# Optimization experiments

Hardware: AMD Instinct MI355X
Metric: run time of the kernel (lower is better)

Reference implementation:

```python
import jax, jax.numpy as jnp
import numpy as np

# Phi-2 config
B, S = 4, 1024            # batch, seq_len (uniform prefill)
T = B * S                 # total tokens
HID = 2560
H = 32                    # attention heads
D = HID // H              # head_size = 80
ROT = int(0.4 * D)        # partial rotary dim = 32
THETA = 10000.0
SCALE = D ** -0.5
NUM_SLOTS = 2 * T


def setup_inputs() -> dict:
    key = jax.random.key(0)
    ks = jax.random.split(key, 6)
    hidden_states = jax.random.normal(ks[0], (T, HID), jnp.float32) * 0.02
    # true rope tables: positions restart per sequence
    pos = jnp.tile(jnp.arange(S, dtype=jnp.float32), B)                 # [T]
    inv_freq = 1.0 / (THETA ** (jnp.arange(0, ROT, 2, dtype=jnp.float32) / ROT))  # [ROT/2]
    freqs = pos[:, None] * inv_freq[None, :]                            # [T, ROT/2]
    cos, sin = jnp.cos(freqs), jnp.sin(freqs)
    slots = jnp.arange(T, dtype=jnp.int32)
    kv_cache_k = jnp.zeros((NUM_SLOTS, H, D), jnp.float32)
    kv_cache_v = jnp.zeros((NUM_SLOTS, H, D), jnp.float32)
    qkv_w = jax.random.normal(ks[1], (3 * HID, HID), jnp.float32) * 0.02
    qkv_b = jax.random.normal(ks[2], (3 * HID,), jnp.float32) * 0.02
    dense_w = jax.random.normal(ks[3], (HID, HID), jnp.float32) * 0.02
    dense_b = jax.random.normal(ks[4], (HID,), jnp.float32) * 0.02
    return {"hidden_states": hidden_states, "cos": cos, "sin": sin, "slots": slots,
            "kv_cache_k": kv_cache_k, "kv_cache_v": kv_cache_v,
            "qkv_w": qkv_w, "qkv_b": qkv_b, "dense_w": dense_w, "dense_b": dense_b}


def _partial_rope(x, cos, sin):
    # x: [T, H, D]; rotate-half rope on the first ROT dims only
    x1 = x[..., : ROT // 2]
    x2 = x[..., ROT // 2 : ROT]
    c = cos[:, None, :]  # [T,1,ROT/2]
    s = sin[:, None, :]
    rot = jnp.concatenate([x1 * c - x2 * s, x1 * s + x2 * c], axis=-1)
    return jnp.concatenate([rot, x[..., ROT:]], axis=-1)


def reference(hidden_states, cos, sin, slots, kv_cache_k, kv_cache_v,
              qkv_w, qkv_b, dense_w, dense_b):
    # fused QKV projection
    qkv = hidden_states @ qkv_w.T + qkv_b                 # [T, 3*HID]
    q = qkv[:, :HID].reshape(T, H, D)
    k = qkv[:, HID:2 * HID].reshape(T, H, D)
    v = qkv[:, 2 * HID:].reshape(T, H, D)
    # partial rotary on q and k
    q = _partial_rope(q, cos, sin)
    k = _partial_rope(k, cos, sin)
    # KV-cache write (reshape_and_cache)
    kc = kv_cache_k.at[slots].set(k)
    vc = kv_cache_v.at[slots].set(v)
    # causal flash-attention (prefill path), uniform seq lengths
    qb = q.reshape(B, S, H, D)
    kb = k.reshape(B, S, H, D)
    vb = v.reshape(B, S, H, D)
    scores = jnp.einsum("bqhd,bkhd->bhqk", qb, kb) * SCALE  # [B,H,S,S]
    causal = jnp.tril(jnp.ones((S, S), bool))
    scores = jnp.where(causal[None, None], scores, jnp.finfo(scores.dtype).min)
    probs = jax.nn.softmax(scores, axis=-1)
    attn = jnp.einsum("bhqk,bkhd->bqhd", probs, vb).reshape(T, HID)
    out = attn @ dense_w.T + dense_b                       # [T, HID]
    return out, kc, vc
```

## Files before the change

kernel.cpp:

```cpp
#include <hip/hip_runtime.h>

#define SEQ    1024
#define NBAT   4
#define TTOK   4096
#define HIDN   2560
#define NQKV   7680
#define NHEAD  32
#define DHEAD  80
#define NSLOT  8192
#define SCALE_F 0.111803398874989485f
#define LOG2E_F 1.4426950408889634f

typedef float  f32x4  __attribute__((ext_vector_type(4)));
typedef __bf16 bf16x8 __attribute__((ext_vector_type(8)));
typedef short  s16x8  __attribute__((ext_vector_type(8)));
typedef short  s16x4  __attribute__((ext_vector_type(4)));
typedef ushort u16x4  __attribute__((ext_vector_type(4)));

typedef __attribute__((address_space(3))) void lds_v;
typedef __attribute__((address_space(1))) void glb_v;

__device__ __forceinline__ void gload16(const void* g, void* l) {
  __builtin_amdgcn_global_load_lds((glb_v*)g, (lds_v*)l, 16, 0, 0);
}

__device__ __forceinline__ f32x4 mfma16(s16x8 a, s16x8 b, f32x4 c) {
  return __builtin_amdgcn_mfma_f32_16x16x32_bf16(
      __builtin_bit_cast(bf16x8, a), __builtin_bit_cast(bf16x8, b), c, 0, 0, 0);
}

__device__ __forceinline__ ushort f2bf(float f) {
  uint u = __builtin_bit_cast(uint, f);
  u += 0x7fffu + ((u >> 16) & 1u);
  return (ushort)(u >> 16);
}
__device__ __forceinline__ float bf2f(ushort h) {
  uint u = (uint)h << 16;
  return __builtin_bit_cast(float, u);
}

__global__ __launch_bounds__(256)
void cvt_f32_bf16(const float* __restrict__ src, ushort* __restrict__ dst, int n) {
  int i = (blockIdx.x * 256 + threadIdx.x) * 4;
  const int stride = gridDim.x * 256 * 4;
  for (; i < n; i += stride) {
    float4 v = *(const float4*)(src + i);
    u16x4 o = { f2bf(v.x), f2bf(v.y), f2bf(v.z), f2bf(v.w) };
    *(u16x4*)(dst + i) = o;
  }
}

template<int OUT_BF16>
__global__ __launch_bounds__(512, 2)
void gemm8p(const ushort* __restrict__ A, const ushort* __restrict__ B,
            const float* __restrict__ bias, void* __restrict__ Cout,
            int M, int N, int K, int GX) {
  __shared__ ushort sA[3][256 * 64];
  __shared__ ushort sB[2][256 * 64];
  const int tid = threadIdx.x;
  const int l   = tid & 63;
  const int w   = tid >> 6;
  const int wm  = w >> 2, wn = w & 3;
  const int r   = l & 15,  g = l >> 4;

  const int nwg = gridDim.x;
  const int cpx = nwg >> 3;
  const int fl  = blockIdx.x;
  const int sw  = (fl & 7) * cpx + (fl >> 3);
  const int bx  = sw % GX, by = sw / GX;
  const int m0  = by * 256, n0 = bx * 256;
  const int NT  = K >> 6;

  const int srow = w * 16 + (l >> 3);
  const int scol = ((l & 7) ^ (l >> 3)) * 8;
  const ushort* Ab = A + (size_t)(m0 + srow) * K + scol;
  const ushort* Bb = B + (size_t)(n0 + srow) * K + scol;
  const size_t r8   = (size_t)8 * K;
  const size_t r128 = (size_t)128 * K;

#define STG_A(t_, h_, buf_) { \
    const ushort* gp = Ab + (size_t)(t_) * 64 + (size_t)(h_) * r128; \
    char* lp = (char*)(&sA[buf_][0]) + ((h_) * 128 + w * 16) * 128; \
    gload16(gp, lp); gload16(gp + r8, lp + 1024); }
#define STG_B(t_, h_, buf_) { \
    const ushort* gp = Bb + (size_t)(t_) * 64 + (size_t)(h_) * r128; \
    char* lp = (char*)(&sB[buf_][0]) + ((h_) * 128 + w * 16) * 128; \
    gload16(gp, lp); gload16(gp + r8, lp + 1024); }

  const int kswz = (r & 7) * 8;
  const int c0 = (g * 8) ^ kswz;
  const int c1 = (32 + g * 8) ^ kswz;
  const int arow = (wm * 128 + r) * 64;
  const int brow = (wn * 64 + r) * 64;

  f32x4 acc[8][4];
#pragma unroll
  for (int m = 0; m < 8; m++)
#pragma unroll
    for (int n = 0; n < 4; n++) { f32x4 z = {0.f,0.f,0.f,0.f}; acc[m][n] = z; }

  STG_A(0, 0, 0); STG_A(0, 1, 0);
  STG_B(0, 0, 0); STG_B(0, 1, 0);
  STG_A(1, 0, 1); STG_A(1, 1, 1);
  asm volatile("s_waitcnt vmcnt(4)" ::: "memory");
  __builtin_amdgcn_sched_barrier(0);
  __builtin_amdgcn_s_barrier();

#define MFMA_Q(q_) \
    __builtin_amdgcn_s_setprio(1); \
    _Pragma("unroll") \
    for (int n = 0; n < 4; n++) { \
      acc[2*(q_)  ][n] = mfma16(x0, b0[n], acc[2*(q_)  ][n]); \
      acc[2*(q_)  ][n] = mfma16(x1, b1[n], acc[2*(q_)  ][n]); \
      acc[2*(q_)+1][n] = mfma16(y0, b0[n], acc[2*(q_)+1][n]); \
      acc[2*(q_)+1][n] = mfma16(y1, b1[n], acc[2*(q_)+1][n]); \
    } \
    __builtin_amdgcn_s_setprio(0);

#define LOAD_A(m0_, m1_) \
    x0 = *(const s16x8*)&cA[arow + (m0_) * 1024 + c0]; \
    x1 = *(const s16x8*)&cA[arow + (m0_) * 1024 + c1]; \
    y0 = *(const s16x8*)&cA[arow + (m1_) * 1024 + c0]; \
    y1 = *(const s16x8*)&cA[arow + (m1_) * 1024 + c1];

  int bA = 0;
#pragma unroll 1
  for (int t = 0; t < NT; ++t) {
    const ushort* cA = &sA[bA][0];
    const ushort* cB = &sB[t & 1][0];
    const int nb = (t & 1) ^ 1;
    int a2 = bA + 2; if (a2 >= 3) a2 -= 3;

    s16x8 b0[4], b1[4], x0, x1, y0, y1;

#pragma unroll
    for (int n = 0; n < 4; n++) {
      b0[n] = *(const s16x8*)&cB[brow + n * 1024 + c0];
      b1[n] = *(const s16x8*)&cB[brow + n * 1024 + c1];
    }
    LOAD_A(0, 1)
    if (t + 1 < NT) STG_B(t + 1, 0, nb);
    __builtin_amdgcn_s_barrier();
    MFMA_Q(0)
    __builtin_amdgcn_s_barrier();

    LOAD_A(2, 3)
    if (t + 1 < NT) STG_B(t + 1, 1, nb);
    __builtin_amdgcn_s_barrier();
    MFMA_Q(1)
    __builtin_amdgcn_s_barrier();

    LOAD_A(4, 5)
    if (t + 2 < NT) STG_A(t + 2, 0, a2);
    __builtin_amdgcn_s_barrier();
    MFMA_Q(2)
    __builtin_amdgcn_s_barrier();

    LOAD_A(6, 7)
    if (t + 2 < NT) STG_A(t + 2, 1, a2);
    __builtin_amdgcn_s_barrier();
    MFMA_Q(3)
    if (t < NT - 2) {
      asm volatile("s_waitcnt vmcnt(4)" ::: "memory");
    } else if (t == NT - 2) {
      asm volatile("s_waitcnt vmcnt(0)" ::: "memory");
    }
    __builtin_amdgcn_sched_barrier(0);
    __builtin_amdgcn_s_barrier();

    bA++; if (bA >= 3) bA = 0;
  }

#pragma unroll
  for (int n = 0; n < 4; n++) {
    const int col = n0 + wn * 64 + n * 16 + r;
    const float bv = bias[col];
#pragma unroll
    for (int m = 0; m < 8; m++) {
      const int row = m0 + wm * 128 + m * 16 + g * 4;
#pragma unroll
      for (int j = 0; j < 4; j++) {
        float v = acc[m][n][j] + bv;
        if (OUT_BF16) ((ushort*)Cout)[(size_t)(row + j) * N + col] = f2bf(v);
        else          ((float*)Cout)[(size_t)(row + j) * N + col] = v;
      }
    }
  }
#undef STG_A
#undef STG_B
#undef MFMA_Q
#undef LOAD_A
}

__global__ __launch_bounds__(256)
void rope_scatter(ushort* __restrict__ qkv, const float* __restrict__ cosp,
                  const float* __restrict__ sinp, const int* __restrict__ slots,
                  float* __restrict__ kc, float* __restrict__ vc) {
  const int t = blockIdx.x;
  const int tid = threadIdx.x;
  __shared__ float cs[16], sn[16];
  if (tid < 16)       cs[tid]      = cosp[t * 16 + tid];
  else if (tid < 32)  sn[tid - 16] = sinp[t * 16 + tid - 16];
  __syncthreads();
  const int slot = slots[t];
  ushort* qrow = qkv + (size_t)t * NQKV;
  float* kcr = kc + (size_t)slot * HIDN;
  float* vcr = vc + (size_t)slot * HIDN;

  for (int idx = tid; idx < 512; idx += 256) {
    int hh = idx >> 4, i = idx & 15;
    ushort* p = qrow + hh * DHEAD + i;
    float x1 = bf2f(p[0]), x2 = bf2f(p[16]);
    float c = cs[i], s = sn[i];
    p[0]  = f2bf(x1 * c - x2 * s);
    p[16] = f2bf(x1 * s + x2 * c);
  }
  for (int idx = tid; idx < 512; idx += 256) {
    int hh = idx >> 4, i = idx & 15;
    ushort* p = qrow + HIDN + hh * DHEAD + i;
    float x1 = bf2f(p[0]), x2 = bf2f(p[16]);
    float c = cs[i], s = sn[i];
    float k1 = x1 * c - x2 * s, k2 = x1 * s + x2 * c;
    p[0]  = f2bf(k1);
    p[16] = f2bf(k2);
    kcr[hh * DHEAD + i]      = k1;
    kcr[hh * DHEAD + i + 16] = k2;
  }
  for (int idx = tid; idx < 1536; idx += 256) {
    int hh = idx / 48, d = 32 + idx % 48;
    kcr[hh * DHEAD + d] = bf2f(qrow[HIDN + hh * DHEAD + d]);
  }
  for (int idx = tid; idx < HIDN; idx += 256) {
    vcr[idx] = bf2f(qrow[2 * HIDN + idx]);
  }
}

__global__ __launch_bounds__(256)
void flags_zero(uint* __restrict__ f) {
  f[blockIdx.x * 256 + threadIdx.x] = 0u;
}
__global__ __launch_bounds__(256)
void flags_mark(const int* __restrict__ slots, uint* __restrict__ f) {
  f[slots[blockIdx.x * 256 + threadIdx.x]] = 1u;
}
__global__ __launch_bounds__(256)
void cache_fill(const float* __restrict__ kin, const float* __restrict__ vin,
                const uint* __restrict__ f,
                float* __restrict__ kout, float* __restrict__ vout) {
  const int row = blockIdx.x;
  if (f[row]) return;
  const float4* ks = (const float4*)(kin + (size_t)row * HIDN);
  const float4* vs = (const float4*)(vin + (size_t)row * HIDN);
  float4* kd = (float4*)(kout + (size_t)row * HIDN);
  float4* vd = (float4*)(vout + (size_t)row * HIDN);
  for (int i = threadIdx.x; i < HIDN / 4; i += 256) { kd[i] = ks[i]; vd[i] = vs[i]; }
}

__global__ __launch_bounds__(512, 4)
void attn_kernel(const ushort* __restrict__ qkv, ushort* __restrict__ attn_out) {
  const int qb = 7 - blockIdx.y;
  const int hb = blockIdx.x;
  const int h = hb & 31, b = hb >> 5;
  __shared__ ushort lsK[64 * 104];
  __shared__ ushort lsVT[80 * 68];
  __shared__ ushort lsP[8][16 * 68];
  const int tid  = threadIdx.x;
  const int lane = tid & 63, w = tid >> 6;
  const int r    = lane & 15, g = lane >> 4;

  {
    int kv = tid >> 3, cp = tid & 7;
    *(uint*)&lsK[kv * 104 + 80 + cp * 2] = 0u;
  }

  const size_t qrow = (size_t)(b * SEQ + qb * 128 + w * 16 + r);
  const ushort* qp = qkv + qrow * NQKV + h * DHEAD;
  s16x8 qf[3];
  qf[0] = *(const s16x8*)(qp + g * 8);
  qf[1] = *(const s16x8*)(qp + 32 + g * 8);
  if (g < 2) qf[2] = *(const s16x8*)(qp + 64 + g * 8);
  else { s16x8 z = {0,0,0,0,0,0,0,0}; qf[2] = z; }

  int off_g[5]; uint off_kv[5];
#pragma unroll
  for (int j = 0; j < 5; j++) {
    int i = tid + j * 512;
    int kv = i / 40, dp = i - kv * 40;
    off_g[j]  = kv * NQKV + dp * 2;
    off_kv[j] = (uint)(kv * 104 + dp * 2) | ((uint)(dp * 2 * 68 + kv) << 16);
  }
  const ushort* kvbase = qkv + (size_t)(b * SEQ) * NQKV + HIDN + h * DHEAD;

  uint kreg[5], vreg[5];
#pragma unroll
  for (int j = 0; j < 5; j++) {
    kreg[j] = *(const uint*)(kvbase + off_g[j]);
    vreg[j] = *(const uint*)(kvbase + off_g[j] + HIDN);
  }

  float m_run[4] = {-1e30f, -1e30f, -1e30f, -1e30f};
  float l_run[4] = {0.f, 0.f, 0.f, 0.f};
  f32x4 acco[5];
#pragma unroll
  for (int nb = 0; nb < 5; nb++) { f32x4 z = {0.f,0.f,0.f,0.f}; acco[nb] = z; }

  const int ntiles = 2 * qb + 2;
  for (int t = 0; t < ntiles; t++) {
#pragma unroll
    for (int j = 0; j < 5; j++) {
      int ok = off_kv[j] & 0xffff, ov = off_kv[j] >> 16;
      *(uint*)&lsK[ok] = kreg[j];
      uint vv = vreg[j];
      lsVT[ov]      = (ushort)(vv & 0xffffu);
      lsVT[ov + 68] = (ushort)(vv >> 16);
    }
    __syncthreads();

    if (t + 1 < ntiles) {
      const ushort* nb_ = kvbase + (size_t)(t + 1) * 64 * NQKV;
#pragma unroll
      for (int j = 0; j < 5; j++) {
        kreg[j] = *(const uint*)(nb_ + off_g[j]);
        vreg[j] = *(const uint*)(nb_ + off_g[j] + HIDN);
      }
    }

    f32x4 sacc[4];
#pragma unroll
    for (int cb = 0; cb < 4; cb++) {
      f32x4 acc = {0.f, 0.f, 0.f, 0.f};
#pragma unroll
      for (int c = 0; c < 3; c++) {
        s16x8 kf = *(const s16x8*)&lsK[(cb * 16 + r) * 104 + c * 32 + g * 8];
        acc = mfma16(qf[c], kf, acc);
      }
      sacc[cb] = acc;
    }

    const bool diag = (t >= 2 * qb);
    const int kv0 = t * 64;
    const int q0  = qb * 128 + w * 16 + g * 4;
#pragma unroll
    for (int cb = 0; cb < 4; cb++)
#pragma unroll
      for (int j = 0; j < 4; j++) {
        float s = sacc[cb][j] * SCALE_F;
        if (diag && (kv0 + cb * 16 + r) > (q0 + j)) s = -1e30f;
        sacc[cb][j] = s;
      }

    float mnew[4], alpha[4], rs[4];
#pragma unroll
    for (int j = 0; j < 4; j++) {
      float m = fmaxf(fmaxf(sacc[0][j], sacc[1][j]), fmaxf(sacc[2][j], sacc[3][j]));
      m = fmaxf(m, __shfl_xor(m, 1));
      m = fmaxf(m, __shfl_xor(m, 2));
      m = fmaxf(m, __shfl_xor(m, 4));
      m = fmaxf(m, __shfl_xor(m, 8));
      mnew[j]  = fmaxf(m_run[j], m);
      alpha[j] = exp2f((m_run[j] - mnew[j]) * LOG2E_F);
      m_run[j] = mnew[j];
      rs[j] = 0.f;
    }

#pragma unroll
    for (int cb = 0; cb < 4; cb++)
#pragma unroll
      for (int j = 0; j < 4; j++) {
        float p = exp2f((sacc[cb][j] - mnew[j]) * LOG2E_F);
        rs[j] += p;
        lsP[w][(g * 4 + j) * 68 + cb * 16 + r] = f2bf(p);
      }

#pragma unroll
    for (int j = 0; j < 4; j++) {
      float v = rs[j];
      v += __shfl_xor(v, 1);
      v += __shfl_xor(v, 2);
      v += __shfl_xor(v, 4);
      v += __shfl_xor(v, 8);
      l_run[j] = l_run[j] * alpha[j] + v;
#pragma unroll
      for (int nb = 0; nb < 5; nb++) acco[nb][j] *= alpha[j];
    }

    s16x8 pa[2];
#pragma unroll
    for (int ch = 0; ch < 2; ch++) {
      s16x4 lo = *(const s16x4*)&lsP[w][r * 68 + ch * 32 + g * 8];
      s16x4 hi = *(const s16x4*)&lsP[w][r * 68 + ch * 32 + g * 8 + 4];
      pa[ch] = __builtin_shufflevector(lo, hi, 0, 1, 2, 3, 4, 5, 6, 7);
    }

#pragma unroll
    for (int nb = 0; nb < 5; nb++)
#pragma unroll
      for (int ch = 0; ch < 2; ch++) {
        s16x4 lo = *(const s16x4*)&lsVT[(nb * 16 + r) * 68 + ch * 32 + g * 8];
        s16x4 hi = *(const s16x4*)&lsVT[(nb * 16 + r) * 68 + ch * 32 + g * 8 + 4];
        s16x8 vf = __builtin_shufflevector(lo, hi, 0, 1, 2, 3, 4, 5, 6, 7);
        acco[nb] = mfma16(pa[ch], vf, acco[nb]);
      }

    __syncthreads();
  }

  const size_t orow = (size_t)(b * SEQ + qb * 128 + w * 16 + g * 4);
#pragma unroll
  for (int j = 0; j < 4; j++) {
    float inv = 1.0f / l_run[j];
#pragma unroll
    for (int nb = 0; nb < 5; nb++)
      attn_out[(orow + j) * HIDN + h * DHEAD + nb * 16 + r] = f2bf(acco[nb][j] * inv);
  }
}

extern "C" void kernel_launch(void* const* d_in, const int* in_sizes, int n_in,
                              void* d_out, int out_size, void* d_ws, size_t ws_size,
                              hipStream_t stream) {
  (void)in_sizes; (void)n_in; (void)out_size; (void)ws_size;
  const float* hs      = (const float*)d_in[0];
  const float* cosp    = (const float*)d_in[1];
  const float* sinp    = (const float*)d_in[2];
  const int*   slots   = (const int*)  d_in[3];
  const float* kck_in  = (const float*)d_in[4];
  const float* kcv_in  = (const float*)d_in[5];
  const float* qkvw    = (const float*)d_in[6];
  const float* qkvb    = (const float*)d_in[7];
  const float* densew  = (const float*)d_in[8];
  const float* denseb  = (const float*)d_in[9];

  float* out    = (float*)d_out;
  float* kc_out = out + (size_t)TTOK * HIDN;
  float* vc_out = kc_out + (size_t)NSLOT * HIDN;

  char* ws = (char*)d_ws;
  ushort* hsb     = (ushort*)(ws);
  ushort* qkvwb   = (ushort*)(ws + 20971520);
  ushort* densewb = (ushort*)(ws + 60293120);
  ushort* qkvb16  = (ushort*)(ws + 73400320);
  ushort* attnb   = (ushort*)(ws + 136314880);
  uint*   flags   = (uint*)ws;

  cvt_f32_bf16<<<2048, 256, 0, stream>>>(hs,     hsb,     TTOK * HIDN);
  cvt_f32_bf16<<<2048, 256, 0, stream>>>(qkvw,   qkvwb,   NQKV * HIDN);
  cvt_f32_bf16<<<1024, 256, 0, stream>>>(densew, densewb, HIDN * HIDN);

  gemm8p<1><<<480, 512, 0, stream>>>(hsb, qkvwb, qkvb, qkvb16, TTOK, NQKV, HIDN, 30);

  flags_zero<<<NSLOT / 256, 256, 0, stream>>>(flags);
  flags_mark<<<TTOK / 256, 256, 0, stream>>>(slots, flags);

  rope_scatter<<<TTOK, 256, 0, stream>>>(qkvb16, cosp, sinp, slots, kc_out, vc_out);

  cache_fill<<<NSLOT, 256, 0, stream>>>(kck_in, kcv_in, flags, kc_out, vc_out);

  attn_kernel<<<dim3(NHEAD * NBAT, SEQ / 128), 512, 0, stream>>>(qkvb16, attnb);

  gemm8p<0><<<160, 512, 0, stream>>>(attnb, densewb, denseb, out, TTOK, HIDN, HIDN, 10);
}
```

Measured before the change: 468.9 us.

## Merge conversion kernels, fold flag marking into rope, use 128-tile dense GEMM

The three fp32-to-bf16 conversion launches and the flag zeroing are merged into one prep kernel, and flag marking moves into rope_scatter, which removes several small launches. The dense output projection switches to a new 128x128-tile, 256-thread GEMM on 640 workgroups instead of 160 large-tile workgroups, which fills more of the CUs. The flags buffer moves to the attention-output region of the workspace, so it is overwritten later by attn_kernel, after cache_fill has already read it. The smaller tiles cost more global and LDS traffic per FLOP.

```diff
diff --git a/kernel.cpp b/kernel.cpp
--- a/kernel.cpp
+++ b/kernel.cpp
@@ -39,14 +39,26 @@
   return __builtin_bit_cast(float, u);
 }
 
+#define NQ_HS  2621440
+#define NQ_QW  4915200
+#define NQ_DW  1638400
+#define NQ_ALL (NQ_HS + NQ_QW + NQ_DW)
 __global__ __launch_bounds__(256)
-void cvt_f32_bf16(const float* __restrict__ src, ushort* __restrict__ dst, int n) {
-  int i = (blockIdx.x * 256 + threadIdx.x) * 4;
-  const int stride = gridDim.x * 256 * 4;
-  for (; i < n; i += stride) {
-    float4 v = *(const float4*)(src + i);
+void prep_kernel(const float* __restrict__ hs, const float* __restrict__ qkvw,
+                 const float* __restrict__ densew,
+                 ushort* __restrict__ hsb, ushort* __restrict__ qkvwb,
+                 ushort* __restrict__ densewb, uint* __restrict__ flags) {
+  const int tid0 = blockIdx.x * 256 + threadIdx.x;
+  if (tid0 < NSLOT) flags[tid0] = 0u;
+  const int stride = gridDim.x * 256;
+  for (int i = tid0; i < NQ_ALL; i += stride) {
+    const float* src; ushort* dst; int q;
+    if (i < NQ_HS)              { src = hs;     dst = hsb;     q = i; }
+    else if (i < NQ_HS + NQ_QW) { src = qkvw;   dst = qkvwb;   q = i - NQ_HS; }
+    else                        { src = densew; dst = densewb; q = i - NQ_HS - NQ_QW; }
+    float4 v = *(const float4*)(src + q * 4);
     u16x4 o = { f2bf(v.x), f2bf(v.y), f2bf(v.z), f2bf(v.w) };
-    *(u16x4*)(dst + i) = o;
+    *(u16x4*)(dst + q * 4) = o;
   }
 }
 
@@ -192,10 +204,145 @@
 #undef LOAD_A
 }
 
+__global__ __launch_bounds__(256, 2)
+void gemm8ph128(const ushort* __restrict__ A, const ushort* __restrict__ B,
+                const float* __restrict__ bias, float* __restrict__ Cout,
+                int M, int N, int K, int GX) {
+  __shared__ ushort sA[3][128 * 64];
+  __shared__ ushort sB[2][128 * 64];
+  const int tid = threadIdx.x;
+  const int l   = tid & 63;
+  const int w   = tid >> 6;
+  const int wm  = w >> 1, wn = w & 1;
+  const int r   = l & 15,  g = l >> 4;
+
+  const int nwg = gridDim.x;
+  const int cpx = nwg >> 3;
+  const int fl  = blockIdx.x;
+  const int sw  = (fl & 7) * cpx + (fl >> 3);
+  const int bx  = sw % GX, by = sw / GX;
+  const int m0  = by * 128, n0 = bx * 128;
+  const int NT  = K >> 6;
+
+  const int srow = w * 16 + (l >> 3);
+  const int scol = ((l & 7) ^ (l >> 3)) * 8;
+  const ushort* Ab = A + (size_t)(m0 + srow) * K + scol;
+  const ushort* Bb = B + (size_t)(n0 + srow) * K + scol;
+  const size_t r8  = (size_t)8 * K;
+  const size_t r64 = (size_t)64 * K;
+
+#define DSTG_A(t_, h_, buf_) { \
+    const ushort* gp = Ab + (size_t)(t_) * 64 + (size_t)(h_) * r64; \
+    char* lp = (char*)(&sA[buf_][0]) + ((h_) * 64 + w * 16) * 128; \
+    gload16(gp, lp); gload16(gp + r8, lp + 1024); }
+#define DSTG_B(t_, h_, buf_) { \
+    const ushort* gp = Bb + (size_t)(t_) * 64 + (size_t)(h_) * r64; \
+    char* lp = (char*)(&sB[buf_][0]) + ((h_) * 64 + w * 16) * 128; \
+    gload16(gp, lp); gload16(gp + r8, lp + 1024); }
+
+  const int kswz = (r & 7) * 8;
+  const int c0 = (g * 8) ^ kswz;
+  const int c1 = (32 + g * 8) ^ kswz;
+  const int arow = (wm * 64 + r) * 64;
+  const int brow = (wn * 64 + r) * 64;
+
+  f32x4 acc[4][4];
+#pragma unroll
+  for (int m = 0; m < 4; m++)
+#pragma unroll
+    for (int n = 0; n < 4; n++) { f32x4 z = {0.f,0.f,0.f,0.f}; acc[m][n] = z; }
+
+  DSTG_A(0, 0, 0); DSTG_A(0, 1, 0);
+  DSTG_B(0, 0, 0); DSTG_B(0, 1, 0);
+  DSTG_A(1, 0, 1); DSTG_A(1, 1, 1);
+  asm volatile("s_waitcnt vmcnt(4)" ::: "memory");
+  __builtin_amdgcn_sched_barrier(0);
+  __builtin_amdgcn_s_barrier();
+
+#define DMFMA(m_) \
+    __builtin_amdgcn_s_setprio(1); \
+    _Pragma("unroll") \
+    for (int n = 0; n < 4; n++) { \
+      acc[m_][n] = mfma16(x0, b0[n], acc[m_][n]); \
+      acc[m_][n] = mfma16(x1, b1[n], acc[m_][n]); \
+    } \
+    __builtin_amdgcn_s_setprio(0);
+
+#define DLOAD_A(m_) \
+    x0 = *(const s16x8*)&cA[arow + (m_) * 1024 + c0]; \
+    x1 = *(const s16x8*)&cA[arow + (m_) * 1024 + c1];
+
+  int bA = 0;
+#pragma unroll 1
+  for (int t = 0; t < NT; ++t) {
+    const ushort* cA = &sA[bA][0];
+    const ushort* cB = &sB[t & 1][0];
+    const int nb = (t & 1) ^ 1;
+    int a2 = bA + 2; if (a2 >= 3) a2 -= 3;
+
+    s16x8 b0[4], b1[4], x0, x1;
+
+#pragma unroll
+    for (int n = 0; n < 4; n++) {
+      b0[n] = *(const s16x8*)&cB[brow + n * 1024 + c0];
+      b1[n] = *(const s16x8*)&cB[brow + n * 1024 + c1];
+    }
+    DLOAD_A(0)
+    if (t + 1 < NT) DSTG_B(t + 1, 0, nb);
+    __builtin_amdgcn_s_barrier();
+    DMFMA(0)
+    __builtin_amdgcn_s_barrier();
+
+    DLOAD_A(1)
+    if (t + 1 < NT) DSTG_B(t + 1, 1, nb);
+    __builtin_amdgcn_s_barrier();
+    DMFMA(1)
+    __builtin_amdgcn_s_barrier();
+
+    DLOAD_A(2)
+    if (t + 2 < NT) DSTG_A(t + 2, 0, a2);
+    __builtin_amdgcn_s_barrier();
+    DMFMA(2)
+    __builtin_amdgcn_s_barrier();
+
+    DLOAD_A(3)
+    if (t + 2 < NT) DSTG_A(t + 2, 1, a2);
+    __builtin_amdgcn_s_barrier();
+    DMFMA(3)
+    if (t < NT - 2) {
+      asm volatile("s_waitcnt vmcnt(4)" ::: "memory");
+    } else if (t == NT - 2) {
+      asm volatile("s_waitcnt vmcnt(0)" ::: "memory");
+    }
+    __builtin_amdgcn_sched_barrier(0);
+    __builtin_amdgcn_s_barrier();
+
+    bA++; if (bA >= 3) bA = 0;
+  }
+
+#pragma unroll
+  for (int n = 0; n < 4; n++) {
+    const int col = n0 + wn * 64 + n * 16 + r;
+    const float bv = bias[col];
+#pragma unroll
+    for (int m = 0; m < 4; m++) {
+      const int row = m0 + wm * 64 + m * 16 + g * 4;
+#pragma unroll
+      for (int j = 0; j < 4; j++)
+        Cout[(size_t)(row + j) * N + col] = acc[m][n][j] + bv;
+    }
+  }
+#undef DSTG_A
+#undef DSTG_B
+#undef DMFMA
+#undef DLOAD_A
+}
+
 __global__ __launch_bounds__(256)
 void rope_scatter(ushort* __restrict__ qkv, const float* __restrict__ cosp,
                   const float* __restrict__ sinp, const int* __restrict__ slots,
-                  float* __restrict__ kc, float* __restrict__ vc) {
+                  float* __restrict__ kc, float* __restrict__ vc,
+                  uint* __restrict__ flags) {
   const int t = blockIdx.x;
   const int tid = threadIdx.x;
   __shared__ float cs[16], sn[16];
@@ -203,6 +350,7 @@
   else if (tid < 32)  sn[tid - 16] = sinp[t * 16 + tid - 16];
   __syncthreads();
   const int slot = slots[t];
+  if (tid == 0) flags[slot] = 1u;
   ushort* qrow = qkv + (size_t)t * NQKV;
   float* kcr = kc + (size_t)slot * HIDN;
   float* vcr = vc + (size_t)slot * HIDN;
@@ -235,14 +383,6 @@
   }
 }
 
-__global__ __launch_bounds__(256)
-void flags_zero(uint* __restrict__ f) {
-  f[blockIdx.x * 256 + threadIdx.x] = 0u;
-}
-__global__ __launch_bounds__(256)
-void flags_mark(const int* __restrict__ slots, uint* __restrict__ f) {
-  f[slots[blockIdx.x * 256 + threadIdx.x]] = 1u;
-}
 __global__ __launch_bounds__(256)
 void cache_fill(const float* __restrict__ kin, const float* __restrict__ vin,
                 const uint* __restrict__ f,
@@ -440,22 +580,17 @@
   ushort* densewb = (ushort*)(ws + 60293120);
   ushort* qkvb16  = (ushort*)(ws + 73400320);
   ushort* attnb   = (ushort*)(ws + 136314880);
-  uint*   flags   = (uint*)ws;
-
-  cvt_f32_bf16<<<2048, 256, 0, stream>>>(hs,     hsb,     TTOK * HIDN);
-  cvt_f32_bf16<<<2048, 256, 0, stream>>>(qkvw,   qkvwb,   NQKV * HIDN);
-  cvt_f32_bf16<<<1024, 256, 0, stream>>>(densew, densewb, HIDN * HIDN);
+  uint*   flags   = (uint*)(ws + 136314880);
+
+  prep_kernel<<<2048, 256, 0, stream>>>(hs, qkvw, densew, hsb, qkvwb, densewb, flags);
 
   gemm8p<1><<<480, 512, 0, stream>>>(hsb, qkvwb, qkvb, qkvb16, TTOK, NQKV, HIDN, 30);
 
-  flags_zero<<<NSLOT / 256, 256, 0, stream>>>(flags);
-  flags_mark<<<TTOK / 256, 256, 0, stream>>>(slots, flags);
-
-  rope_scatter<<<TTOK, 256, 0, stream>>>(qkvb16, cosp, sinp, slots, kc_out, vc_out);
+  rope_scatter<<<TTOK, 256, 0, stream>>>(qkvb16, cosp, sinp, slots, kc_out, vc_out, flags);
 
   cache_fill<<<NSLOT, 256, 0, stream>>>(kck_in, kcv_in, flags, kc_out, vc_out);
 
   attn_kernel<<<dim3(NHEAD * NBAT, SEQ / 128), 512, 0, stream>>>(qkvb16, attnb);
 
-  gemm8p<0><<<160, 512, 0, stream>>>(attnb, densewb, denseb, out, TTOK, HIDN, HIDN, 10);
-}
+  gemm8ph128<<<640, 256, 0, stream>>>(attnb, densewb, denseb, out, TTOK, HIDN, HIDN, 20);
+}
```

Result: slower. 483.1 us (+3.0%).
